# Performance work log

Measured on AMD Instinct MI355X. Metric: run time of the kernel, lower is better.

## Reference

```python
import jax, jax.numpy as jnp
import numpy as np

NUM_GRAPHS = 256  # static batch size (= batch_indices.max()+1 by construction)
EMBED = 32
HIDDEN = 256
DEPTH = 10


def setup_inputs() -> dict:
    key = jax.random.key(0)
    ks = jax.random.split(key, 16)
    N, M = 8192, 16384
    atom_features = jax.random.randint(ks[0], (N,), 0, 200, dtype=jnp.int32)
    bond_features = jax.random.randint(ks[1], (M,), 0, 10, dtype=jnp.int32)
    adjacency_matrix = jax.random.randint(ks[2], (N, N), 0, 2, dtype=jnp.int32)
    batch_indices = jnp.sort(jax.random.randint(ks[3], (N,), 0, NUM_GRAPHS, dtype=jnp.int32))
    s = 0.05
    atom_emb_table = jax.random.normal(ks[4], (200, EMBED), jnp.float32) * s
    bond_emb_table = jax.random.normal(ks[5], (10, EMBED), jnp.float32) * s
    msg_W = jax.random.normal(ks[6], (DEPTH, HIDDEN, 2 * EMBED), jnp.float32) * s
    msg_b = jax.random.normal(ks[7], (DEPTH, HIDDEN), jnp.float32) * s
    gru_Wih = jax.random.normal(ks[8], (DEPTH, 3 * EMBED, HIDDEN), jnp.float32) * s
    gru_Whh = jax.random.normal(ks[9], (DEPTH, 3 * EMBED, EMBED), jnp.float32) * s
    gru_bih = jax.random.normal(ks[10], (DEPTH, 3 * EMBED), jnp.float32) * s
    gru_bhh = jax.random.normal(ks[11], (DEPTH, 3 * EMBED), jnp.float32) * s
    pool_W = jax.random.normal(ks[12], (HIDDEN, EMBED), jnp.float32) * s
    pool_b = jax.random.normal(ks[13], (HIDDEN,), jnp.float32) * s
    return dict(atom_features=atom_features, bond_features=bond_features,
                adjacency_matrix=adjacency_matrix, batch_indices=batch_indices,
                atom_emb_table=atom_emb_table, bond_emb_table=bond_emb_table,
                msg_W=msg_W, msg_b=msg_b, gru_Wih=gru_Wih, gru_Whh=gru_Whh,
                gru_bih=gru_bih, gru_bhh=gru_bhh, pool_W=pool_W, pool_b=pool_b)


def _gru_step(x, h, Wih, Whh, bih, bhh):
    # single-step torch-style GRU cell: x [N,HIDDEN], h [N,EMBED]
    gi = x @ Wih.T + bih                      # [N, 3E]
    gh = h @ Whh.T + bhh                      # [N, 3E]
    i_r, i_z, i_n = jnp.split(gi, 3, axis=-1)
    h_r, h_z, h_n = jnp.split(gh, 3, axis=-1)
    r = jax.nn.sigmoid(i_r + h_r)
    z = jax.nn.sigmoid(i_z + h_z)
    n = jnp.tanh(i_n + r * h_n)
    return (1.0 - z) * n + z * h


def reference(atom_features, bond_features, adjacency_matrix, batch_indices,
              atom_emb_table, bond_emb_table, msg_W, msg_b,
              gru_Wih, gru_Whh, gru_bih, gru_bhh, pool_W, pool_b):
    h = atom_emb_table[atom_features]                      # [N, E]
    A = (adjacency_matrix != 0).astype(h.dtype)            # [N, N]
    deg = A.sum(axis=-1, keepdims=True)                    # [N, 1]
    inv_deg = 1.0 / jnp.maximum(deg, 1.0)
    has_nei = deg > 0
    for d in range(DEPTH):
        # mean over neighbors of Linear(concat(self, nei)) == affine in (self, mean_nei)
        nei_mean = (A @ h) * inv_deg                       # [N, E]
        W_self = msg_W[d][:, :EMBED]                       # [H, E]
        W_nei = msg_W[d][:, EMBED:]                        # [H, E]
        msg = h @ W_self.T + nei_mean @ W_nei.T + msg_b[d]  # [N, H]
        msg = jnp.where(has_nei, msg, 0.0)                 # zero message if no neighbors
        h = _gru_step(msg, h, gru_Wih[d], gru_Whh[d], gru_bih[d], gru_bhh[d])
        # dropout is identity in eval mode
    # segment-mean pooling over graphs (zeros for empty graphs)
    sums = jax.ops.segment_sum(h, batch_indices, num_segments=NUM_GRAPHS)      # [B, E]
    counts = jax.ops.segment_sum(jnp.ones((h.shape[0],), h.dtype), batch_indices,
                                 num_segments=NUM_GRAPHS)[:, None]             # [B, 1]
    graph_mean = jnp.where(counts > 0, sums / jnp.maximum(counts, 1.0), 0.0)
    graph_embeddings = graph_mean @ pool_W.T + pool_b                          # [B, H]
    bond_embeddings = bond_emb_table[bond_features]                            # [M, E]
    return h, bond_embeddings, graph_embeddings
```

## Files before the change

### kernel.cpp

```cpp
#include <hip/hip_runtime.h>
#include <stdint.h>

#define N_ATOMS 8192
#define EMBED   32
#define DEPTHN  10

typedef short bf16x8 __attribute__((ext_vector_type(8)));
typedef float f32x4  __attribute__((ext_vector_type(4)));

__device__ __forceinline__ unsigned short f2bf(float f){
    unsigned u = __builtin_bit_cast(unsigned, f);
    u = u + 0x7FFFu + ((u >> 16) & 1u);
    return (unsigned short)(u >> 16);
}

__global__ __launch_bounds__(256) void k_preA(const int* __restrict__ A,
                                              unsigned long long* __restrict__ mask,
                                              int row0)
{
    const int i = row0 + blockIdx.x;
    const int t = threadIdx.x, w = t >> 6, l = t & 63;
    const int* row = A + (size_t)i * N_ATOMS;
    __shared__ unsigned long long lm[128];
    #pragma unroll
    for (int k = 0; k < 32; ++k){
        int j = k*256 + t;
        unsigned long long m = __ballot(row[j] != 0);
        if (l == 0) lm[k*4 + w] = m;
    }
    __syncthreads();
    if (t < 128) mask[(size_t)i*128 + t] = lm[t];
}

__global__ __launch_bounds__(256) void k_pack(const unsigned* __restrict__ maskRM,
                                              unsigned* __restrict__ mP,
                                              float* __restrict__ deg,
                                              float* __restrict__ invdeg)
{
    const int grp = blockIdx.x, t = threadIdx.x;
    __shared__ unsigned lm[16*260];
    __shared__ int red[256];
    #pragma unroll
    for (int s = 0; s < 16; ++s)
        lm[s*260 + t] = maskRM[(size_t)grp*4096 + s*256 + t];
    __syncthreads();
    {
        int r = t >> 4, seg = t & 15, cnt = 0;
        #pragma unroll
        for (int k = 0; k < 16; ++k) cnt += __popc(lm[r*260 + seg*16 + k]);
        red[t] = cnt; __syncthreads();
        if (t < 16){
            int s = 0;
            #pragma unroll
            for (int k = 0; k < 16; ++k) s += red[t*16 + k];
            deg[grp*16 + t] = (float)s;
            invdeg[grp*16 + t] = 1.f / fmaxf((float)s, 1.f);
        }
    }
    unsigned* out = mP + (size_t)grp*4096;
    #pragma unroll
    for (int s = 0; s < 16; ++s){
        int W = s*256 + t;
        out[W] = lm[(W & 15)*260 + (W >> 4)];
    }
}

__global__ __launch_bounds__(256) void k_setup(
    const int* __restrict__ af, const float* __restrict__ atom_emb,
    const float* __restrict__ msgW, const float* __restrict__ msgb,
    const float* __restrict__ Wih, const float* __restrict__ bih,
    float* __restrict__ hA, unsigned short* __restrict__ hP,
    float* __restrict__ Wc, float* __restrict__ bc)
{
    const int blk = blockIdx.x, t = threadIdx.x;
    if (blk < 1024){
        int idx = blk*256 + t;
        int i = idx >> 5, e = idx & 31;
        float v = atom_emb[af[i]*EMBED + e];
        hA[idx] = v;
        int g = i >> 5, qd = (i >> 3) & 3, j8 = i & 7;
        hP[(size_t)((g*2 + (e>>4))*64 + qd*16 + (e&15))*8 + j8] = f2bf(v);
    } else if (blk < 1264){
        int o = (blk-1024)*256 + t;
        int d = o / 6144, r = o % 6144, g = r >> 6, e = r & 63;
        const float* wi = Wih  + (size_t)(d*96 + g)*256;
        const float* mw = msgW + (size_t)d*256*64 + e;
        float acc = 0.f;
        for (int hh = 0; hh < 256; ++hh) acc += wi[hh] * mw[hh*64];
        Wc[o] = acc;
    } else {
        int o = (blk-1264)*256 + t;
        if (o < 960){
            int d = o / 96;
            const float* wi = Wih + (size_t)o*256;
            const float* mb = msgb + d*256;
            float acc = 0.f;
            for (int hh = 0; hh < 256; ++hh) acc += wi[hh] * mb[hh];
            bc[o] = acc + bih[o];
        }
    }
}

__global__ __launch_bounds__(256) void k_nei(const unsigned short* __restrict__ hP,
                                             const unsigned* __restrict__ mP,
                                             float* __restrict__ neipart)
{
    const int rb = blockIdx.x & 63;
    const int q  = blockIdx.x >> 6;
    const int t = threadIdx.x, w = t >> 6, lane = t & 63;
    const int n = lane & 15, quad = lane >> 4;
    const int rt0 = rb*8 + w*2;

    f32x4 a00 = {0.f,0.f,0.f,0.f};
    f32x4 a01 = {0.f,0.f,0.f,0.f};
    f32x4 a10 = {0.f,0.f,0.f,0.f};
    f32x4 a11 = {0.f,0.f,0.f,0.f};

    const unsigned* m0 = mP + (size_t)rt0*4096 + n;
    const unsigned* m1 = m0 + 4096;
    #pragma unroll 4
    for (int kk = 0; kk < 32; ++kk){
        const int g = q*32 + kk;
        union { uint4 u; bf16x8 v; } b0, b1;
        b0.u = *(const uint4*)&hP[(size_t)((g*2+0)*64 + lane)*8];
        b1.u = *(const uint4*)&hP[(size_t)((g*2+1)*64 + lane)*8];
        unsigned by0 = (m0[g*16] >> (quad*8)) & 0xFFu;
        unsigned by1 = (m1[g*16] >> (quad*8)) & 0xFFu;
        union { unsigned u[4]; bf16x8 v; } af0, af1;
        af0.u[0] = ((by0 & 1u)  ? 0x3F80u : 0u) | ((by0 & 2u)   ? 0x3F800000u : 0u);
        af0.u[1] = ((by0 & 4u)  ? 0x3F80u : 0u) | ((by0 & 8u)   ? 0x3F800000u : 0u);
        af0.u[2] = ((by0 & 16u) ? 0x3F80u : 0u) | ((by0 & 32u)  ? 0x3F800000u : 0u);
        af0.u[3] = ((by0 & 64u) ? 0x3F80u : 0u) | ((by0 & 128u) ? 0x3F800000u : 0u);
        af1.u[0] = ((by1 & 1u)  ? 0x3F80u : 0u) | ((by1 & 2u)   ? 0x3F800000u : 0u);
        af1.u[1] = ((by1 & 4u)  ? 0x3F80u : 0u) | ((by1 & 8u)   ? 0x3F800000u : 0u);
        af1.u[2] = ((by1 & 16u) ? 0x3F80u : 0u) | ((by1 & 32u)  ? 0x3F800000u : 0u);
        af1.u[3] = ((by1 & 64u) ? 0x3F80u : 0u) | ((by1 & 128u) ? 0x3F800000u : 0u);
        a00 = __builtin_amdgcn_mfma_f32_16x16x32_bf16(af0.v, b0.v, a00, 0, 0, 0);
        a01 = __builtin_amdgcn_mfma_f32_16x16x32_bf16(af0.v, b1.v, a01, 0, 0, 0);
        a10 = __builtin_amdgcn_mfma_f32_16x16x32_bf16(af1.v, b0.v, a10, 0, 0, 0);
        a11 = __builtin_amdgcn_mfma_f32_16x16x32_bf16(af1.v, b1.v, a11, 0, 0, 0);
    }
    float* outp = neipart + (size_t)q * N_ATOMS * EMBED;
    #pragma unroll
    for (int r = 0; r < 4; ++r){
        int row0 = rt0*16 + quad*4 + r;
        int row1 = row0 + 16;
        outp[(size_t)row0*EMBED + n]      = a00[r];
        outp[(size_t)row0*EMBED + 16 + n] = a01[r];
        outp[(size_t)row1*EMBED + n]      = a10[r];
        outp[(size_t)row1*EMBED + 16 + n] = a11[r];
    }
}

__global__ __launch_bounds__(256) void k_gru(
    const float* __restrict__ hin, float* __restrict__ hout,
    const float* __restrict__ neipart,
    const float* __restrict__ invdeg, const float* __restrict__ deg,
    const float* __restrict__ Wc, const float* __restrict__ bc,
    const float* __restrict__ bihf, const float* __restrict__ bhhf,
    const float* __restrict__ Whhf,
    unsigned short* __restrict__ hP, float* __restrict__ out0, int last)
{
    __shared__ float xs[32][68];
    const int t = threadIdx.x, blk = blockIdx.x;
    {
        float4 v = *(const float4*)&hin[(size_t)blk*1024 + t*4];
        int a = t >> 3, e = (t*4) & 31;
        *(float4*)&xs[a][e] = v;
        float4 s = {0.f,0.f,0.f,0.f};
        #pragma unroll
        for (int q = 0; q < 8; ++q){
            float4 v2 = *(const float4*)&neipart[(size_t)q*N_ATOMS*EMBED + blk*1024 + t*4];
            s.x += v2.x; s.y += v2.y; s.z += v2.z; s.w += v2.w;
        }
        *(float4*)&xs[a][32 + e] = s;
    }
    __syncthreads();

    const int a32 = t & 31, grp = t >> 5;
    const int atom = blk*32 + a32;
    const float idg = invdeg[atom];
    const bool nz = deg[atom] > 0.f;
    float x[64];
    #pragma unroll
    for (int r = 0; r < 16; ++r){
        float4 v = *(const float4*)&xs[a32][r*4];
        x[r*4+0]=v.x; x[r*4+1]=v.y; x[r*4+2]=v.z; x[r*4+3]=v.w;
    }
    #pragma unroll
    for (int e = 32; e < 64; ++e) x[e] *= idg;

    const int g = atom >> 5, qd = (atom >> 3) & 3, j8 = atom & 7;
    #pragma unroll
    for (int jj = 0; jj < 4; ++jj){
        const int j = grp*4 + jj;
        const float* wr = Wc + j*64;
        const float* wz = Wc + (32+j)*64;
        const float* wn = Wc + (64+j)*64;
        float gr=0.f, gz=0.f, gn=0.f;
        #pragma unroll
        for (int e = 0; e < 64; ++e){ gr += wr[e]*x[e]; gz += wz[e]*x[e]; gn += wn[e]*x[e]; }
        if (nz){ gr += bc[j]; gz += bc[32+j]; gn += bc[64+j]; }
        else   { gr  = bihf[j]; gz = bihf[32+j]; gn = bihf[64+j]; }
        const float* vr = Whhf + j*32;
        const float* vz = Whhf + (32+j)*32;
        const float* vn = Whhf + (64+j)*32;
        float hr=bhhf[j], hz=bhhf[32+j], hn=bhhf[64+j];
        #pragma unroll
        for (int e = 0; e < 32; ++e){ hr += vr[e]*x[e]; hz += vz[e]*x[e]; hn += vn[e]*x[e]; }
        float rg = 1.f/(1.f + expf(-(gr+hr)));
        float zg = 1.f/(1.f + expf(-(gz+hz)));
        float ng = tanhf(gn + rg*hn);
        float hnew = (1.f - zg)*ng + zg*x[j];
        hout[(size_t)atom*EMBED + j] = hnew;
        hP[(size_t)((g*2 + (j>>4))*64 + qd*16 + (j&15))*8 + j8] = f2bf(hnew);
        if (last) out0[(size_t)atom*EMBED + j] = hnew;
    }
}

__global__ __launch_bounds__(256) void k_bond(const int* __restrict__ bfeat,
                                              const float* __restrict__ bondf,
                                              float* __restrict__ out1)
{
    int idx = blockIdx.x*256 + threadIdx.x;
    out1[idx] = bondf[bfeat[idx >> 5]*EMBED + (idx & 31)];
}

__global__ __launch_bounds__(256) void k_pool(
    const float* __restrict__ h, const int* __restrict__ batch,
    const float* __restrict__ poolW, const float* __restrict__ poolb,
    float* __restrict__ out2)
{
    const int b = blockIdx.x, t = threadIdx.x;
    int lo, hi;
    { int l = 0, r = N_ATOMS; while (l < r){ int m = (l+r)>>1; if (batch[m] < b)   l = m+1; else r = m; } lo = l; }
    { int l = 0, r = N_ATOMS; while (l < r){ int m = (l+r)>>1; if (batch[m] < b+1) l = m+1; else r = m; } hi = l; }
    const int cnt = hi - lo;
    __shared__ float ps[8][32];
    __shared__ float mean[32];
    const int e = t & 31, g = t >> 5;
    float acc = 0.f;
    for (int a = lo + g; a < hi; a += 8) acc += h[(size_t)a*EMBED + e];
    ps[g][e] = acc; __syncthreads();
    if (t < 32){
        float s = 0.f;
        #pragma unroll
        for (int gg = 0; gg < 8; ++gg) s += ps[gg][t];
        mean[t] = (cnt > 0) ? s / (float)cnt : 0.f;
    }
    __syncthreads();
    float emb = poolb[t];
    #pragma unroll
    for (int ee = 0; ee < 32; ++ee) emb += mean[ee] * poolW[t*32 + ee];
    out2[b*256 + t] = emb;
}

extern "C" void kernel_launch(void* const* d_in, const int* in_sizes, int n_in,
                              void* d_out, int out_size, void* d_ws, size_t ws_size,
                              hipStream_t stream)
{
    (void)in_sizes; (void)n_in; (void)out_size;
    const int* af   = (const int*)d_in[0];
    const int* bfe  = (const int*)d_in[1];
    const int* A    = (const int*)d_in[2];
    const int* bidx = (const int*)d_in[3];
    const float* atom_emb = (const float*)d_in[4];
    const float* bond_emb = (const float*)d_in[5];
    const float* msgW  = (const float*)d_in[6];
    const float* msgb  = (const float*)d_in[7];
    const float* Wih   = (const float*)d_in[8];
    const float* Whh   = (const float*)d_in[9];
    const float* bih   = (const float*)d_in[10];
    const float* bhh   = (const float*)d_in[11];
    const float* poolW = (const float*)d_in[12];
    const float* poolb = (const float*)d_in[13];

    float* out0 = (float*)d_out;
    float* out1 = out0 + 262144;
    float* out2 = out1 + 524288;

    float* deg    = out2;
    float* invdeg = out2 + 8192;

    unsigned long long* maskRM;
    unsigned*       mP;
    float*          hA; float* hB; float* Wc; float* bc; float* neipart;
    unsigned short* hP;
    const int wsok = (ws_size >= (size_t)33554432) ? 1 : 0;
    if (wsok){
        char* W = (char*)d_ws;
        maskRM  = (unsigned long long*)(W + 0);
        mP      = (unsigned*)(W + 8388608);
        hP      = (unsigned short*)(W + 16777216);
        hA      = (float*)(W + 17825792);
        hB      = (float*)(W + 18874368);
        Wc      = (float*)(W + 19922944);
        bc      = (float*)(W + 20185088);
        neipart = (float*)(W + 20971520);
        k_preA<<<dim3(8192), dim3(256), 0, stream>>>(A, maskRM, 0);
    } else {
        char* Ab = (char*)d_in[2];
        hA      = (float*)(Ab + 0);
        hB      = (float*)(Ab + 1048576);
        hP      = (unsigned short*)(Ab + 2097152);
        Wc      = (float*)(Ab + 2621440);
        bc      = (float*)(Ab + 2867200);
        neipart = (float*)(Ab + 4194304);
        mP      = (unsigned*)(Ab + 13631488);
        maskRM  = (unsigned long long*)(Ab + 260046848);
        k_preA<<<dim3(1),    dim3(256), 0, stream>>>(A, maskRM, 8191);
        k_preA<<<dim3(7),    dim3(256), 0, stream>>>(A, maskRM, 8184);
        k_preA<<<dim3(248),  dim3(256), 0, stream>>>(A, maskRM, 7936);
        k_preA<<<dim3(7936), dim3(256), 0, stream>>>(A, maskRM, 0);
    }
    k_pack<<<dim3(512), dim3(256), 0, stream>>>((const unsigned*)maskRM, mP,
        deg, invdeg);
    k_setup<<<dim3(1268), dim3(256), 0, stream>>>(af, atom_emb, msgW, msgb,
        Wih, bih, hA, hP, Wc, bc);

    float* hin = hA; float* hout = hB;
    for (int d = 0; d < DEPTHN; ++d){
        k_nei<<<dim3(512), dim3(256), 0, stream>>>(hP, mP, neipart);
        k_gru<<<dim3(256), dim3(256), 0, stream>>>(hin, hout, neipart, invdeg, deg,
            Wc + d*6144, bc + d*96, bih + d*96, bhh + d*96, Whh + d*3072,
            hP, out0, (d == DEPTHN-1) ? 1 : 0);
        float* tmp = hin; hin = hout; hout = tmp;
    }
    k_bond<<<dim3(2048), dim3(256), 0, stream>>>(bfe, bond_emb, out1);
    k_pool<<<dim3(256), dim3(256), 0, stream>>>(hin, bidx, poolW, poolb, out2);
}
```

Before: 759.5 us.

## Fuse bond gather into setup, LUT mask expansion, halve GRU block size

Three independent changes. The bond embedding gather moves into the setup kernel as extra blocks, which removes one kernel launch. In k_nei, the per-bit select chain that expands mask bytes into bf16 1.0/0.0 values is replaced by a 16-entry shared-memory lookup table, at the cost of LDS reads and a __syncthreads. k_gru now processes 16 atoms per block instead of 32 across 512 blocks, with half the threads loading h and half summing the neighbor partials, to spread work over more CUs.

```diff
diff --git a/kernel.cpp b/kernel.cpp
--- a/kernel.cpp
+++ b/kernel.cpp
@@ -70,7 +70,9 @@
     const float* __restrict__ msgW, const float* __restrict__ msgb,
     const float* __restrict__ Wih, const float* __restrict__ bih,
     float* __restrict__ hA, unsigned short* __restrict__ hP,
-    float* __restrict__ Wc, float* __restrict__ bc)
+    float* __restrict__ Wc, float* __restrict__ bc,
+    const int* __restrict__ bfeat, const float* __restrict__ bondf,
+    float* __restrict__ out1)
 {
     const int blk = blockIdx.x, t = threadIdx.x;
     if (blk < 1024){
@@ -88,7 +90,7 @@
         float acc = 0.f;
         for (int hh = 0; hh < 256; ++hh) acc += wi[hh] * mw[hh*64];
         Wc[o] = acc;
-    } else {
+    } else if (blk < 1268){
         int o = (blk-1264)*256 + t;
         if (o < 960){
             int d = o / 96;
@@ -98,6 +100,9 @@
             for (int hh = 0; hh < 256; ++hh) acc += wi[hh] * mb[hh];
             bc[o] = acc + bih[o];
         }
+    } else {
+        int idx = (blk-1268)*256 + t;
+        out1[idx] = bondf[bfeat[idx >> 5]*EMBED + (idx & 31)];
     }
 }
 
@@ -105,9 +110,16 @@
                                              const unsigned* __restrict__ mP,
                                              float* __restrict__ neipart)
 {
+    __shared__ uint2 lut[16];
     const int rb = blockIdx.x & 63;
     const int q  = blockIdx.x >> 6;
     const int t = threadIdx.x, w = t >> 6, lane = t & 63;
+    if (t < 16){
+        unsigned lo = ((t & 1) ? 0x3F80u : 0u) | ((t & 2) ? 0x3F800000u : 0u);
+        unsigned hi = ((t & 4) ? 0x3F80u : 0u) | ((t & 8) ? 0x3F800000u : 0u);
+        lut[t] = make_uint2(lo, hi);
+    }
+    __syncthreads();
     const int n = lane & 15, quad = lane >> 4;
     const int rt0 = rb*8 + w*2;
 
@@ -126,15 +138,11 @@
         b1.u = *(const uint4*)&hP[(size_t)((g*2+1)*64 + lane)*8];
         unsigned by0 = (m0[g*16] >> (quad*8)) & 0xFFu;
         unsigned by1 = (m1[g*16] >> (quad*8)) & 0xFFu;
-        union { unsigned u[4]; bf16x8 v; } af0, af1;
-        af0.u[0] = ((by0 & 1u)  ? 0x3F80u : 0u) | ((by0 & 2u)   ? 0x3F800000u : 0u);
-        af0.u[1] = ((by0 & 4u)  ? 0x3F80u : 0u) | ((by0 & 8u)   ? 0x3F800000u : 0u);
-        af0.u[2] = ((by0 & 16u) ? 0x3F80u : 0u) | ((by0 & 32u)  ? 0x3F800000u : 0u);
-        af0.u[3] = ((by0 & 64u) ? 0x3F80u : 0u) | ((by0 & 128u) ? 0x3F800000u : 0u);
-        af1.u[0] = ((by1 & 1u)  ? 0x3F80u : 0u) | ((by1 & 2u)   ? 0x3F800000u : 0u);
-        af1.u[1] = ((by1 & 4u)  ? 0x3F80u : 0u) | ((by1 & 8u)   ? 0x3F800000u : 0u);
-        af1.u[2] = ((by1 & 16u) ? 0x3F80u : 0u) | ((by1 & 32u)  ? 0x3F800000u : 0u);
-        af1.u[3] = ((by1 & 64u) ? 0x3F80u : 0u) | ((by1 & 128u) ? 0x3F800000u : 0u);
+        union { uint2 d[2]; bf16x8 v; } af0, af1;
+        af0.d[0] = lut[by0 & 15u];
+        af0.d[1] = lut[by0 >> 4];
+        af1.d[0] = lut[by1 & 15u];
+        af1.d[1] = lut[by1 >> 4];
         a00 = __builtin_amdgcn_mfma_f32_16x16x32_bf16(af0.v, b0.v, a00, 0, 0, 0);
         a01 = __builtin_amdgcn_mfma_f32_16x16x32_bf16(af0.v, b1.v, a01, 0, 0, 0);
         a10 = __builtin_amdgcn_mfma_f32_16x16x32_bf16(af1.v, b0.v, a10, 0, 0, 0);
@@ -161,30 +169,33 @@
     const float* __restrict__ Whhf,
     unsigned short* __restrict__ hP, float* __restrict__ out0, int last)
 {
-    __shared__ float xs[32][68];
+    __shared__ float xs[16][68];
     const int t = threadIdx.x, blk = blockIdx.x;
-    {
-        float4 v = *(const float4*)&hin[(size_t)blk*1024 + t*4];
+    if (t < 128){
+        float4 v = *(const float4*)&hin[(size_t)blk*512 + t*4];
         int a = t >> 3, e = (t*4) & 31;
         *(float4*)&xs[a][e] = v;
+    } else {
+        int u = t - 128;
+        int a = u >> 3, e = (u*4) & 31;
         float4 s = {0.f,0.f,0.f,0.f};
         #pragma unroll
         for (int q = 0; q < 8; ++q){
-            float4 v2 = *(const float4*)&neipart[(size_t)q*N_ATOMS*EMBED + blk*1024 + t*4];
+            float4 v2 = *(const float4*)&neipart[(size_t)q*N_ATOMS*EMBED + blk*512 + u*4];
             s.x += v2.x; s.y += v2.y; s.z += v2.z; s.w += v2.w;
         }
         *(float4*)&xs[a][32 + e] = s;
     }
     __syncthreads();
 
-    const int a32 = t & 31, grp = t >> 5;
-    const int atom = blk*32 + a32;
+    const int a = t & 15, p = t >> 4;
+    const int atom = blk*16 + a;
     const float idg = invdeg[atom];
     const bool nz = deg[atom] > 0.f;
     float x[64];
     #pragma unroll
     for (int r = 0; r < 16; ++r){
-        float4 v = *(const float4*)&xs[a32][r*4];
+        float4 v = *(const float4*)&xs[a][r*4];
         x[r*4+0]=v.x; x[r*4+1]=v.y; x[r*4+2]=v.z; x[r*4+3]=v.w;
     }
     #pragma unroll
@@ -192,8 +203,8 @@
 
     const int g = atom >> 5, qd = (atom >> 3) & 3, j8 = atom & 7;
     #pragma unroll
-    for (int jj = 0; jj < 4; ++jj){
-        const int j = grp*4 + jj;
+    for (int jj = 0; jj < 2; ++jj){
+        const int j = p*2 + jj;
         const float* wr = Wc + j*64;
         const float* wz = Wc + (32+j)*64;
         const float* wn = Wc + (64+j)*64;
@@ -216,14 +227,6 @@
         hP[(size_t)((g*2 + (j>>4))*64 + qd*16 + (j&15))*8 + j8] = f2bf(hnew);
         if (last) out0[(size_t)atom*EMBED + j] = hnew;
     }
-}
-
-__global__ __launch_bounds__(256) void k_bond(const int* __restrict__ bfeat,
-                                              const float* __restrict__ bondf,
-                                              float* __restrict__ out1)
-{
-    int idx = blockIdx.x*256 + threadIdx.x;
-    out1[idx] = bondf[bfeat[idx >> 5]*EMBED + (idx & 31)];
 }
 
 __global__ __launch_bounds__(256) void k_pool(
@@ -315,17 +318,16 @@
     }
     k_pack<<<dim3(512), dim3(256), 0, stream>>>((const unsigned*)maskRM, mP,
         deg, invdeg);
-    k_setup<<<dim3(1268), dim3(256), 0, stream>>>(af, atom_emb, msgW, msgb,
-        Wih, bih, hA, hP, Wc, bc);
+    k_setup<<<dim3(3316), dim3(256), 0, stream>>>(af, atom_emb, msgW, msgb,
+        Wih, bih, hA, hP, Wc, bc, bfe, bond_emb, out1);
 
     float* hin = hA; float* hout = hB;
     for (int d = 0; d < DEPTHN; ++d){
         k_nei<<<dim3(512), dim3(256), 0, stream>>>(hP, mP, neipart);
-        k_gru<<<dim3(256), dim3(256), 0, stream>>>(hin, hout, neipart, invdeg, deg,
+        k_gru<<<dim3(512), dim3(256), 0, stream>>>(hin, hout, neipart, invdeg, deg,
             Wc + d*6144, bc + d*96, bih + d*96, bhh + d*96, Whh + d*3072,
             hP, out0, (d == DEPTHN-1) ? 1 : 0);
         float* tmp = hin; hin = hout; hout = tmp;
     }
-    k_bond<<<dim3(2048), dim3(256), 0, stream>>>(bfe, bond_emb, out1);
     k_pool<<<dim3(256), dim3(256), 0, stream>>>(hin, bidx, poolW, poolb, out2);
 }
```

Measured after the change: 727.8 us. 4.2% less time.
